# Kernel tuning notes

Hardware: AMD Instinct MI355X
Metric: run time of the kernel (lower is better)

Reference implementation:

```python
import jax, jax.numpy as jnp
import numpy as np
import math

B, S, D, H = 2, 2048, 1024, 16
DK = D // H


def setup_inputs() -> dict:
    key = jax.random.key(0)
    ks = jax.random.split(key, 8)
    s = 1.0 / math.sqrt(D)
    inp = {
        "query": jax.random.normal(ks[0], (B, S, D), jnp.float32),
        "key": jax.random.normal(ks[1], (B, S, D), jnp.float32),
        "value": jax.random.normal(ks[2], (B, S, D), jnp.float32),
        # causal mask: (1, 1, S, S), 1 where attention allowed
        "mask": jnp.tril(jnp.ones((S, S), jnp.int32))[None, None, :, :],
        "Wq": jax.random.normal(ks[3], (D, D), jnp.float32) * s,
        "Wk": jax.random.normal(ks[4], (D, D), jnp.float32) * s,
        "Wv": jax.random.normal(ks[5], (D, D), jnp.float32) * s,
        "Wo": jax.random.normal(ks[6], (D, D), jnp.float32) * s,
    }
    return inp


def reference(query, key, value, mask, Wq, Wk, Wv, Wo):
    # nn.Linear(bias=False): y = x @ W.T
    def proj_heads(x, W):
        y = jnp.einsum("bsd,ed->bse", x, W)          # (B,S,D)
        return y.reshape(B, -1, H, DK).transpose(0, 2, 1, 3)  # (B,H,S,DK)

    q = proj_heads(query, Wq)
    k = proj_heads(key, Wk)
    v = proj_heads(value, Wv)

    scale = jnp.asarray(math.sqrt(DK), q.dtype)
    scores = jnp.einsum("bhqd,bhkd->bhqk", q, k) / scale  # (B,H,S,S)
    scores = jnp.where(mask == 0, -jnp.inf, scores)
    attn = jax.nn.softmax(scores, axis=-1)
    # dropout p=0.0 (eval): identity
    out = jnp.einsum("bhqk,bhkd->bhqd", attn, v)          # (B,H,S,DK)
    concat = out.transpose(0, 2, 1, 3).reshape(B, -1, D)  # (B,S,D)
    return jnp.einsum("bsd,ed->bse", concat, Wo)
```

## Files before the change

kernel.cpp:

```cpp
#include <hip/hip_runtime.h>
#include <hip/hip_bf16.h>

#define B_ 2
#define S_ 2048
#define D_ 1024
#define H_ 16
#define DK_ 64

typedef __hip_bfloat16 bf16;
typedef __attribute__((ext_vector_type(8))) short bf16x8;
typedef __attribute__((ext_vector_type(4))) short bf16x4;
typedef __attribute__((ext_vector_type(4))) float f32x4;

#define GLDS16(g, l)                                                     \
    __builtin_amdgcn_global_load_lds(                                    \
        (const __attribute__((address_space(1))) void*)(g),              \
        (__attribute__((address_space(3))) void*)(l), 16, 0, 0)

#define MFMA_K32(a, b, c) __builtin_amdgcn_mfma_f32_16x16x32_bf16(a, b, c, 0, 0, 0)
#define MFMA_K16(a, b, c) __builtin_amdgcn_mfma_f32_16x16x16bf16_1k(a, b, c, 0, 0, 0)
#define EXP2F(x) __builtin_amdgcn_exp2f(x)

__global__ __launch_bounds__(256) void cvt_all(
    const float* __restrict__ q, const float* __restrict__ k, const float* __restrict__ v,
    const float* __restrict__ w0, const float* __restrict__ w1,
    const float* __restrict__ w2, const float* __restrict__ w3,
    bf16* __restrict__ oq, bf16* __restrict__ ok, bf16* __restrict__ ov,
    bf16* __restrict__ o0, bf16* __restrict__ o1, bf16* __restrict__ o2,
    bf16* __restrict__ o3) {
    int bid = blockIdx.x;
    const float* src; bf16* dst; int base;
    if      (bid < 2048) { src = q;  dst = oq; base = bid; }
    else if (bid < 4096) { src = k;  dst = ok; base = bid - 2048; }
    else if (bid < 6144) { src = v;  dst = ov; base = bid - 4096; }
    else if (bid < 6656) { src = w0; dst = o0; base = bid - 6144; }
    else if (bid < 7168) { src = w1; dst = o1; base = bid - 6656; }
    else if (bid < 7680) { src = w2; dst = o2; base = bid - 7168; }
    else                 { src = w3; dst = o3; base = bid - 7680; }
    int i = (base * 256 + threadIdx.x) * 8;
    float4 a = *(const float4*)(src + i);
    float4 b = *(const float4*)(src + i + 4);
    __align__(16) bf16 o[8];
    o[0] = __float2bfloat16(a.x); o[1] = __float2bfloat16(a.y);
    o[2] = __float2bfloat16(a.z); o[3] = __float2bfloat16(a.w);
    o[4] = __float2bfloat16(b.x); o[5] = __float2bfloat16(b.y);
    o[6] = __float2bfloat16(b.z); o[7] = __float2bfloat16(b.w);
    *(bf16x8*)(dst + i) = *(const bf16x8*)o;
}

__device__ __forceinline__ void proj_loop32(const bf16* __restrict__ X,
                                            const bf16* __restrict__ W,
                                            int m0, int n0, bf16* As, bf16* Bs,
                                            f32x4 (&acc)[4][4]) {
    const int K = D_;
    const int tid = threadIdx.x;
    const int lane = tid & 63, wave = tid >> 6;
    const int lm = lane & 15, quad = lane >> 4;
    const int wr = wave >> 1, wc = wave & 1;

    auto stage = [&](int t, int bf) {
        int k0 = t * 32;
        bf16* Ab = As + bf * (128 * 32);
        bf16* Bb = Bs + bf * (128 * 32);
#pragma unroll
        for (int i = 0; i < 2; ++i) {
            int s = i * 256 + tid;
            int row = s >> 2, c = (s & 3) ^ (row & 3);
            GLDS16(X + (size_t)(m0 + row) * K + k0 + c * 8, Ab + s * 8);
        }
#pragma unroll
        for (int i = 0; i < 2; ++i) {
            int s = i * 256 + tid;
            int row = s >> 2, c = (s & 3) ^ (row & 3);
            GLDS16(W + (size_t)(n0 + row) * K + k0 + c * 8, Bb + s * 8);
        }
    };

    stage(0, 0);
    for (int t = 0; t < K / 32; ++t) {
        __syncthreads();
        if (t + 1 < K / 32) stage(t + 1, (t + 1) & 1);
        const bf16* Ab = As + (t & 1) * (128 * 32);
        const bf16* Bb = Bs + (t & 1) * (128 * 32);
        bf16x8 aF[4], bF[4];
#pragma unroll
        for (int mt = 0; mt < 4; ++mt) {
            int row = wr * 64 + mt * 16 + lm;
            aF[mt] = *(const bf16x8*)(Ab + row * 32 + ((quad ^ (row & 3)) * 8));
        }
#pragma unroll
        for (int nt = 0; nt < 4; ++nt) {
            int row = wc * 64 + nt * 16 + lm;
            bF[nt] = *(const bf16x8*)(Bb + row * 32 + ((quad ^ (row & 3)) * 8));
        }
#pragma unroll
        for (int mt = 0; mt < 4; ++mt)
#pragma unroll
            for (int nt = 0; nt < 4; ++nt)
                acc[mt][nt] = MFMA_K32(aF[mt], bF[nt], acc[mt][nt]);
    }
}

__global__ __launch_bounds__(256) void proj_qkv(
    const bf16* __restrict__ qx, const bf16* __restrict__ kx, const bf16* __restrict__ vx,
    const bf16* __restrict__ wq, const bf16* __restrict__ wk, const bf16* __restrict__ wv,
    bf16* __restrict__ qb, bf16* __restrict__ kb, bf16* __restrict__ vtb) {
    __shared__ __align__(16) bf16 As[2 * 128 * 32];
    __shared__ __align__(16) bf16 Bs[2 * 128 * 32];
    const int L = (int)blockIdx.x;
    const int tile = (L & 7) * 96 + (L >> 3);
    const int z = tile >> 8;
    const int rem = tile & 255;
    const int n0 = (rem & 7) * 128;
    const int m0 = (rem >> 3) * 128;
    const bf16* X = (z == 0) ? qx : (z == 1) ? kx : vx;
    const bf16* W = (z == 0) ? wq : (z == 1) ? wk : wv;
    f32x4 acc[4][4] = {};
    proj_loop32(X, W, m0, n0, As, Bs, acc);

    const int lane = threadIdx.x & 63, wave = threadIdx.x >> 6;
    const int lm = lane & 15, quad = lane >> 4;
    const int wr = wave >> 1, wc = wave & 1;
#pragma unroll
    for (int mt = 0; mt < 4; ++mt) {
        int mbase = m0 + wr * 64 + mt * 16 + quad * 4;
#pragma unroll
        for (int nt = 0; nt < 4; ++nt) {
            int n = n0 + wc * 64 + nt * 16 + lm;
            if (z == 2) {
                int b = mbase >> 11, s = mbase & (S_ - 1);
                unsigned short u[4];
#pragma unroll
                for (int r = 0; r < 4; ++r) {
                    bf16 hv = __float2bfloat16(acc[mt][nt][r]);
                    u[r] = *(unsigned short*)&hv;
                }
                ushort4 pk = {u[0], u[1], u[2], u[3]};
                *(ushort4*)(vtb + ((size_t)(b * 1024 + n) * S_ + s)) = pk;
            } else {
                bf16* Y = z ? kb : qb;
#pragma unroll
                for (int r = 0; r < 4; ++r)
                    Y[(size_t)(mbase + r) * D_ + n] = __float2bfloat16(acc[mt][nt][r]);
            }
        }
    }
}

__global__ __launch_bounds__(256) void proj_o(const bf16* __restrict__ X,
                                              const bf16* __restrict__ W,
                                              float* __restrict__ Y) {
    __shared__ __align__(16) bf16 As[2 * 64 * 32];
    __shared__ __align__(16) bf16 Bs[2 * 128 * 32];
    const int L = (int)blockIdx.x;
    const int tile = (L & 7) * 64 + (L >> 3);
    const int n0 = (tile & 7) * 128;
    const int m0 = (tile >> 3) * 64;

    const int K = D_;
    const int tid = threadIdx.x;
    const int lane = tid & 63, wave = tid >> 6;
    const int lm = lane & 15, quad = lane >> 4;
    const int wr = wave >> 1, wc = wave & 1;

    f32x4 acc[2][4] = {};

    auto stage = [&](int t, int bf) {
        int k0 = t * 32;
        bf16* Ab = As + bf * (64 * 32);
        bf16* Bb = Bs + bf * (128 * 32);
        {
            int s = tid;
            int row = s >> 2, c = (s & 3) ^ (row & 3);
            GLDS16(X + (size_t)(m0 + row) * K + k0 + c * 8, Ab + s * 8);
        }
#pragma unroll
        for (int i = 0; i < 2; ++i) {
            int s = i * 256 + tid;
            int row = s >> 2, c = (s & 3) ^ (row & 3);
            GLDS16(W + (size_t)(n0 + row) * K + k0 + c * 8, Bb + s * 8);
        }
    };

    stage(0, 0);
    for (int t = 0; t < K / 32; ++t) {
        __syncthreads();
        if (t + 1 < K / 32) stage(t + 1, (t + 1) & 1);
        const bf16* Ab = As + (t & 1) * (64 * 32);
        const bf16* Bb = Bs + (t & 1) * (128 * 32);
        bf16x8 aF[2], bF[4];
#pragma unroll
        for (int mt = 0; mt < 2; ++mt) {
            int row = wr * 32 + mt * 16 + lm;
            aF[mt] = *(const bf16x8*)(Ab + row * 32 + ((quad ^ (row & 3)) * 8));
        }
#pragma unroll
        for (int nt = 0; nt < 4; ++nt) {
            int row = wc * 64 + nt * 16 + lm;
            bF[nt] = *(const bf16x8*)(Bb + row * 32 + ((quad ^ (row & 3)) * 8));
        }
#pragma unroll
        for (int mt = 0; mt < 2; ++mt)
#pragma unroll
            for (int nt = 0; nt < 4; ++nt)
                acc[mt][nt] = MFMA_K32(aF[mt], bF[nt], acc[mt][nt]);
    }

#pragma unroll
    for (int mt = 0; mt < 2; ++mt) {
        int mbase = m0 + wr * 32 + mt * 16 + quad * 4;
#pragma unroll
        for (int nt = 0; nt < 4; ++nt) {
            int n = n0 + wc * 64 + nt * 16 + lm;
#pragma unroll
            for (int r = 0; r < 4; ++r)
                Y[(size_t)(mbase + r) * D_ + n] = acc[mt][nt][r];
        }
    }
}

__global__ __launch_bounds__(1024, 4) void attn_kernel(const bf16* __restrict__ Q,
                                                       const bf16* __restrict__ Kb,
                                                       const bf16* __restrict__ VT,
                                                       bf16* __restrict__ O) {
    __shared__ __align__(16) bf16 smem[4 * 128 * 64];
    bf16* ktb0 = smem;
    bf16* vtb0 = smem + 2 * 128 * 64;

    const int tid = threadIdx.x;
    const int lane = tid & 63, wave = tid >> 6;
    const int ws = wave & 7, jh = wave >> 3;
    const int lm = lane & 15, quad = lane >> 4;
    const int f = (int)blockIdx.x;
    const int cls = f & 7;
    const int t = f >> 3;
    const int p = t >> 2;
    const int combo = cls + 8 * (t & 3);
    const int b = combo >> 4, h = combo & 15;
    const int qiA = p, qiB = 15 - p;
    const int q0A = qiA * 128 + ws * 16;
    const int q0B = qiB * 128 + ws * 16;

    const size_t bhoff = (size_t)b * S_ * D_ + (size_t)h * DK_;
    const bf16* vtg = VT + ((size_t)b * 1024 + h * DK_) * S_;

    const bf16* qpA = Q + bhoff + (size_t)(q0A + lm) * D_ + quad * 8;
    bf16x8 aqA0 = *(const bf16x8*)(qpA);
    bf16x8 aqA1 = *(const bf16x8*)(qpA + 32);
    const bf16* qpB = Q + bhoff + (size_t)(q0B + lm) * D_ + quad * 8;
    bf16x8 aqB0 = *(const bf16x8*)(qpB);
    bf16x8 aqB1 = *(const bf16x8*)(qpB + 32);

    f32x4 oaccA[4] = {}, oaccB[4] = {};
    float lsumA = 0.f, lsumB = 0.f;
    const float cexp = 0.125f * 1.44269504f;

    auto stage = [&](int i, int bf) {
        int j0s = i * 128;
        {
            int s = tid;
            int j = s >> 3, c = (s & 7) ^ (j & 7);
            GLDS16(Kb + bhoff + (size_t)(j0s + j) * D_ + c * 8,
                   ktb0 + bf * (128 * 64) + s * 8);
        }
        {
            int s = tid;
            int d = s >> 4, c = (s & 15) ^ (d & 15);
            GLDS16(vtg + (size_t)d * S_ + j0s + c * 8,
                   vtb0 + bf * (64 * 128) + s * 8);
        }
    };

    auto dochunk = [&](bf16x8 bk0, bf16x8 bk1, const bf16x4 (&bv)[4], bool mk,
                       bf16x8 aq0, bf16x8 aq1, f32x4 (&oacc)[4], float& lsum) {
        f32x4 z = {};
        z = MFMA_K32(bk0, aq0, z);
        z = MFMA_K32(bk1, aq1, z);
        bf16x4 pa;
        float rs = 0.f;
#pragma unroll
        for (int r = 0; r < 4; ++r) {
            float pv = EXP2F(z[r] * cexp);
            if (mk && (quad * 4 + r > lm)) pv = 0.f;
            rs += pv;
            bf16 hv = __float2bfloat16(pv);
            pa[r] = *(short*)&hv;
        }
        lsum += rs;
#pragma unroll
        for (int dt = 0; dt < 4; ++dt)
            oacc[dt] = MFMA_K16(pa, bv[dt], oacc[dt]);
    };

    const int nt = qiB + 1;
    stage(0, 0);

    for (int i = 0; i < nt; ++i) {
        __syncthreads();
        if (i + 1 < nt) stage(i + 1, (i + 1) & 1);
        const bf16* ktb = ktb0 + (i & 1) * (128 * 64);
        const bf16* vtl = vtb0 + (i & 1) * (64 * 128);

#pragma unroll
        for (int stl = 0; stl < 4; ++stl) {
            int sg = jh * 4 + stl;
            bool actB = (i < qiB) || (sg <= ws);
            bool mkB  = (i == qiB) && (sg == ws);
            bool actA = (i < qiA) || ((i == qiA) && (sg <= ws));
            bool mkA  = (i == qiA) && (sg == ws);
            if (!actB && !actA) continue;

            int j = sg * 16 + lm;
            bf16x8 bk0 = *(const bf16x8*)(ktb + (((j << 3) | (quad ^ (j & 7))) * 8));
            bf16x8 bk1 = *(const bf16x8*)(ktb + (((j << 3) | ((4 + quad) ^ (j & 7))) * 8));
            bf16x4 bv[4];
#pragma unroll
            for (int dt = 0; dt < 4; ++dt) {
                int d = dt * 16 + lm;
                int cl = sg * 2 + (quad >> 1);
                bv[dt] = *(const bf16x4*)(vtl + d * 128 +
                                          ((cl ^ (d & 15)) * 8 + (quad & 1) * 4));
            }
            if (actB) dochunk(bk0, bk1, bv, mkB, aqB0, aqB1, oaccB, lsumB);
            if (actA) dochunk(bk0, bk1, bv, mkA, aqA0, aqA1, oaccA, lsumA);
        }
    }

    __syncthreads();
    float* red = (float*)smem;
    const int rbase = (ws * 64 + lane) * 17;

    auto reduce_finish = [&](f32x4 (&oacc)[4], float lsum, int q0) {
        if (jh == 1) {
#pragma unroll
            for (int dt = 0; dt < 4; ++dt)
#pragma unroll
                for (int r = 0; r < 4; ++r)
                    red[rbase + dt * 4 + r] = oacc[dt][r];
            red[rbase + 16] = lsum;
        }
        __syncthreads();
        if (jh == 0) {
#pragma unroll
            for (int dt = 0; dt < 4; ++dt)
#pragma unroll
                for (int r = 0; r < 4; ++r)
                    oacc[dt][r] += red[rbase + dt * 4 + r];
            float l = lsum + red[rbase + 16];
            l += __shfl_xor(l, 16, 64);
            l += __shfl_xor(l, 32, 64);
#pragma unroll
            for (int r = 0; r < 4; ++r) {
                float inv = 1.f / __shfl(l, quad * 4 + r, 64);
                int qrow = q0 + quad * 4 + r;
#pragma unroll
                for (int dt = 0; dt < 4; ++dt) {
                    int d = dt * 16 + lm;
                    O[bhoff + (size_t)qrow * D_ + d] =
                        __float2bfloat16(oacc[dt][r] * inv);
                }
            }
        }
        __syncthreads();
    };
    reduce_finish(oaccB, lsumB, q0B);
    reduce_finish(oaccA, lsumA, q0A);
}

extern "C" void kernel_launch(void* const* d_in, const int* in_sizes, int n_in,
                              void* d_out, int out_size, void* d_ws, size_t ws_size,
                              hipStream_t stream) {
    const float* q_in = (const float*)d_in[0];
    const float* k_in = (const float*)d_in[1];
    const float* v_in = (const float*)d_in[2];
    const float* Wq_f = (const float*)d_in[4];
    const float* Wk_f = (const float*)d_in[5];
    const float* Wv_f = (const float*)d_in[6];
    const float* Wo_f = (const float*)d_in[7];
    float* out = (float*)d_out;

    const size_t NEL = (size_t)B_ * S_ * D_;
    const size_t WEL = (size_t)D_ * D_;
    bf16* p = (bf16*)d_ws;
    bf16* qx = p;  p += NEL;
    bf16* kx = p;  p += NEL;
    bf16* vx = p;  p += NEL;
    bf16* wq = p;  p += WEL;
    bf16* wk = p;  p += WEL;
    bf16* wv = p;  p += WEL;
    bf16* wo = p;  p += WEL;
    bf16* qb = p;  p += NEL;
    bf16* kb = p;  p += NEL;
    bf16* vtb = p; p += NEL;
    bf16* cb = p;  p += NEL;

    cvt_all<<<8192, 256, 0, stream>>>(q_in, k_in, v_in, Wq_f, Wk_f, Wv_f, Wo_f,
                                      qx, kx, vx, wq, wk, wv, wo);

    proj_qkv<<<dim3(768), 256, 0, stream>>>(qx, kx, vx, wq, wk, wv, qb, kb, vtb);

    attn_kernel<<<dim3(256), 1024, 0, stream>>>(qb, kb, vtb, cb);

    dim3 gproj(D_ / 128, (B_ * S_) / 128);
    proj_o<<<dim3(512), 256, 0, stream>>>(cb, wo, out);
}
```

Before: 211.7 us.

## Triple-buffer projection GEMM loads with explicit vmcnt waits and raw barriers

The projection GEMM main loop moves from double to triple buffering of its LDS tiles, prefetching two K-steps ahead. Each iteration waits with a partial s_waitcnt vmcnt and a raw s_barrier instead of a full __syncthreads, so loads for the next step can stay in flight while the current tile is consumed. The output projection kernel now shares the templated loop. This adds LDS use per block and relies on the hand-set vmcnt counts matching the number of loads issued per stage.

```diff
diff --git a/kernel.cpp b/kernel.cpp
--- a/kernel.cpp
+++ b/kernel.cpp
@@ -48,10 +48,16 @@
     *(bf16x8*)(dst + i) = *(const bf16x8*)o;
 }
 
-__device__ __forceinline__ void proj_loop32(const bf16* __restrict__ X,
-                                            const bf16* __restrict__ W,
-                                            int m0, int n0, bf16* As, bf16* Bs,
-                                            f32x4 (&acc)[4][4]) {
+template <int MROWS>
+__device__ __forceinline__ void proj_loop(const bf16* __restrict__ X,
+                                          const bf16* __restrict__ W,
+                                          int m0, int n0, bf16* As, bf16* Bs,
+                                          f32x4 (&acc)[MROWS / 32][4]) {
+    constexpr int MT = MROWS / 32;
+    constexpr int ASZ = MROWS * 32;
+    constexpr int BSZ = 128 * 32;
+    constexpr int NA = (MROWS * 4) / 256;
+    constexpr int NT = D_ / 32;
     const int K = D_;
     const int tid = threadIdx.x;
     const int lane = tid & 63, wave = tid >> 6;
@@ -60,10 +66,10 @@
 
     auto stage = [&](int t, int bf) {
         int k0 = t * 32;
-        bf16* Ab = As + bf * (128 * 32);
-        bf16* Bb = Bs + bf * (128 * 32);
-#pragma unroll
-        for (int i = 0; i < 2; ++i) {
+        bf16* Ab = As + bf * ASZ;
+        bf16* Bb = Bs + bf * BSZ;
+#pragma unroll
+        for (int i = 0; i < NA; ++i) {
             int s = i * 256 + tid;
             int row = s >> 2, c = (s & 3) ^ (row & 3);
             GLDS16(X + (size_t)(m0 + row) * K + k0 + c * 8, Ab + s * 8);
@@ -77,15 +83,26 @@
     };
 
     stage(0, 0);
-    for (int t = 0; t < K / 32; ++t) {
-        __syncthreads();
-        if (t + 1 < K / 32) stage(t + 1, (t + 1) & 1);
-        const bf16* Ab = As + (t & 1) * (128 * 32);
-        const bf16* Bb = Bs + (t & 1) * (128 * 32);
-        bf16x8 aF[4], bF[4];
-#pragma unroll
-        for (int mt = 0; mt < 4; ++mt) {
-            int row = wr * 64 + mt * 16 + lm;
+    stage(1, 1);
+    for (int t = 0; t < NT; ++t) {
+        if (t + 1 < NT) {
+            if constexpr (MROWS == 128) {
+                asm volatile("s_waitcnt vmcnt(4)" ::: "memory");
+            } else {
+                asm volatile("s_waitcnt vmcnt(3)" ::: "memory");
+            }
+        } else {
+            asm volatile("s_waitcnt vmcnt(0)" ::: "memory");
+        }
+        __builtin_amdgcn_sched_barrier(0);
+        __builtin_amdgcn_s_barrier();
+        if (t + 2 < NT) stage(t + 2, (t + 2) % 3);
+        const bf16* Ab = As + (t % 3) * ASZ;
+        const bf16* Bb = Bs + (t % 3) * BSZ;
+        bf16x8 aF[MT], bF[4];
+#pragma unroll
+        for (int mt = 0; mt < MT; ++mt) {
+            int row = wr * (MROWS / 2) + mt * 16 + lm;
             aF[mt] = *(const bf16x8*)(Ab + row * 32 + ((quad ^ (row & 3)) * 8));
         }
 #pragma unroll
@@ -94,7 +111,7 @@
             bF[nt] = *(const bf16x8*)(Bb + row * 32 + ((quad ^ (row & 3)) * 8));
         }
 #pragma unroll
-        for (int mt = 0; mt < 4; ++mt)
+        for (int mt = 0; mt < MT; ++mt)
 #pragma unroll
             for (int nt = 0; nt < 4; ++nt)
                 acc[mt][nt] = MFMA_K32(aF[mt], bF[nt], acc[mt][nt]);
@@ -105,8 +122,8 @@
     const bf16* __restrict__ qx, const bf16* __restrict__ kx, const bf16* __restrict__ vx,
     const bf16* __restrict__ wq, const bf16* __restrict__ wk, const bf16* __restrict__ wv,
     bf16* __restrict__ qb, bf16* __restrict__ kb, bf16* __restrict__ vtb) {
-    __shared__ __align__(16) bf16 As[2 * 128 * 32];
-    __shared__ __align__(16) bf16 Bs[2 * 128 * 32];
+    __shared__ __align__(16) bf16 As[3 * 128 * 32];
+    __shared__ __align__(16) bf16 Bs[3 * 128 * 32];
     const int L = (int)blockIdx.x;
     const int tile = (L & 7) * 96 + (L >> 3);
     const int z = tile >> 8;
@@ -116,7 +133,7 @@
     const bf16* X = (z == 0) ? qx : (z == 1) ? kx : vx;
     const bf16* W = (z == 0) ? wq : (z == 1) ? wk : wv;
     f32x4 acc[4][4] = {};
-    proj_loop32(X, W, m0, n0, As, Bs, acc);
+    proj_loop<128>(X, W, m0, n0, As, Bs, acc);
 
     const int lane = threadIdx.x & 63, wave = threadIdx.x >> 6;
     const int lm = lane & 15, quad = lane >> 4;
@@ -150,62 +167,18 @@
 __global__ __launch_bounds__(256) void proj_o(const bf16* __restrict__ X,
                                               const bf16* __restrict__ W,
                                               float* __restrict__ Y) {
-    __shared__ __align__(16) bf16 As[2 * 64 * 32];
-    __shared__ __align__(16) bf16 Bs[2 * 128 * 32];
+    __shared__ __align__(16) bf16 As[3 * 64 * 32];
+    __shared__ __align__(16) bf16 Bs[3 * 128 * 32];
     const int L = (int)blockIdx.x;
     const int tile = (L & 7) * 64 + (L >> 3);
     const int n0 = (tile & 7) * 128;
     const int m0 = (tile >> 3) * 64;
-
-    const int K = D_;
-    const int tid = threadIdx.x;
-    const int lane = tid & 63, wave = tid >> 6;
+    f32x4 acc[2][4] = {};
+    proj_loop<64>(X, W, m0, n0, As, Bs, acc);
+
+    const int lane = threadIdx.x & 63, wave = threadIdx.x >> 6;
     const int lm = lane & 15, quad = lane >> 4;
     const int wr = wave >> 1, wc = wave & 1;
-
-    f32x4 acc[2][4] = {};
-
-    auto stage = [&](int t, int bf) {
-        int k0 = t * 32;
-        bf16* Ab = As + bf * (64 * 32);
-        bf16* Bb = Bs + bf * (128 * 32);
-        {
-            int s = tid;
-            int row = s >> 2, c = (s & 3) ^ (row & 3);
-            GLDS16(X + (size_t)(m0 + row) * K + k0 + c * 8, Ab + s * 8);
-        }
-#pragma unroll
-        for (int i = 0; i < 2; ++i) {
-            int s = i * 256 + tid;
-            int row = s >> 2, c = (s & 3) ^ (row & 3);
-            GLDS16(W + (size_t)(n0 + row) * K + k0 + c * 8, Bb + s * 8);
-        }
-    };
-
-    stage(0, 0);
-    for (int t = 0; t < K / 32; ++t) {
-        __syncthreads();
-        if (t + 1 < K / 32) stage(t + 1, (t + 1) & 1);
-        const bf16* Ab = As + (t & 1) * (64 * 32);
-        const bf16* Bb = Bs + (t & 1) * (128 * 32);
-        bf16x8 aF[2], bF[4];
-#pragma unroll
-        for (int mt = 0; mt < 2; ++mt) {
-            int row = wr * 32 + mt * 16 + lm;
-            aF[mt] = *(const bf16x8*)(Ab + row * 32 + ((quad ^ (row & 3)) * 8));
-        }
-#pragma unroll
-        for (int nt = 0; nt < 4; ++nt) {
-            int row = wc * 64 + nt * 16 + lm;
-            bF[nt] = *(const bf16x8*)(Bb + row * 32 + ((quad ^ (row & 3)) * 8));
-        }
-#pragma unroll
-        for (int mt = 0; mt < 2; ++mt)
-#pragma unroll
-            for (int nt = 0; nt < 4; ++nt)
-                acc[mt][nt] = MFMA_K32(aF[mt], bF[nt], acc[mt][nt]);
-    }
-
 #pragma unroll
     for (int mt = 0; mt < 2; ++mt) {
         int mbase = m0 + wr * 32 + mt * 16 + quad * 4;
@@ -401,6 +374,5 @@
 
     attn_kernel<<<dim3(256), 1024, 0, stream>>>(qb, kb, vtb, cb);
 
-    dim3 gproj(D_ / 128, (B_ * S_) / 128);
     proj_o<<<dim3(512), 256, 0, stream>>>(cb, wo, out);
 }
```

Result: slower. 221.6 us (+4.7%).

## Fuse fp32-to-bf16 conversion into QKV projection loads and attention prologue

Applied to the files above, without the earlier changes.

Removes the separate cvt_all kernel. The QKV projection now reads fp32 inputs and weights directly through register-staged loads, converts them to bf16 and writes them into LDS, replacing the global_load_lds DMA path. The Wo conversion moves into the attention kernel prologue, where 256 blocks of 1024 threads cover the 1M weight elements. This saves a launch and the bf16 round-trip through global memory, at the cost of doubled fp32 read bytes per GEMM tile (reread across N-tiles) and register-staged rather than async LDS loads.

```diff
diff --git a/kernel.cpp b/kernel.cpp
--- a/kernel.cpp
+++ b/kernel.cpp
@@ -21,89 +21,18 @@
 #define MFMA_K16(a, b, c) __builtin_amdgcn_mfma_f32_16x16x16bf16_1k(a, b, c, 0, 0, 0)
 #define EXP2F(x) __builtin_amdgcn_exp2f(x)
 
-__global__ __launch_bounds__(256) void cvt_all(
-    const float* __restrict__ q, const float* __restrict__ k, const float* __restrict__ v,
-    const float* __restrict__ w0, const float* __restrict__ w1,
-    const float* __restrict__ w2, const float* __restrict__ w3,
-    bf16* __restrict__ oq, bf16* __restrict__ ok, bf16* __restrict__ ov,
-    bf16* __restrict__ o0, bf16* __restrict__ o1, bf16* __restrict__ o2,
-    bf16* __restrict__ o3) {
-    int bid = blockIdx.x;
-    const float* src; bf16* dst; int base;
-    if      (bid < 2048) { src = q;  dst = oq; base = bid; }
-    else if (bid < 4096) { src = k;  dst = ok; base = bid - 2048; }
-    else if (bid < 6144) { src = v;  dst = ov; base = bid - 4096; }
-    else if (bid < 6656) { src = w0; dst = o0; base = bid - 6144; }
-    else if (bid < 7168) { src = w1; dst = o1; base = bid - 6656; }
-    else if (bid < 7680) { src = w2; dst = o2; base = bid - 7168; }
-    else                 { src = w3; dst = o3; base = bid - 7680; }
-    int i = (base * 256 + threadIdx.x) * 8;
-    float4 a = *(const float4*)(src + i);
-    float4 b = *(const float4*)(src + i + 4);
-    __align__(16) bf16 o[8];
-    o[0] = __float2bfloat16(a.x); o[1] = __float2bfloat16(a.y);
-    o[2] = __float2bfloat16(a.z); o[3] = __float2bfloat16(a.w);
-    o[4] = __float2bfloat16(b.x); o[5] = __float2bfloat16(b.y);
-    o[6] = __float2bfloat16(b.z); o[7] = __float2bfloat16(b.w);
-    *(bf16x8*)(dst + i) = *(const bf16x8*)o;
-}
-
-__device__ __forceinline__ void proj_loop32(const bf16* __restrict__ X,
-                                            const bf16* __restrict__ W,
-                                            int m0, int n0, bf16* As, bf16* Bs,
-                                            f32x4 (&acc)[4][4]) {
-    const int K = D_;
-    const int tid = threadIdx.x;
-    const int lane = tid & 63, wave = tid >> 6;
-    const int lm = lane & 15, quad = lane >> 4;
-    const int wr = wave >> 1, wc = wave & 1;
-
-    auto stage = [&](int t, int bf) {
-        int k0 = t * 32;
-        bf16* Ab = As + bf * (128 * 32);
-        bf16* Bb = Bs + bf * (128 * 32);
-#pragma unroll
-        for (int i = 0; i < 2; ++i) {
-            int s = i * 256 + tid;
-            int row = s >> 2, c = (s & 3) ^ (row & 3);
-            GLDS16(X + (size_t)(m0 + row) * K + k0 + c * 8, Ab + s * 8);
-        }
-#pragma unroll
-        for (int i = 0; i < 2; ++i) {
-            int s = i * 256 + tid;
-            int row = s >> 2, c = (s & 3) ^ (row & 3);
-            GLDS16(W + (size_t)(n0 + row) * K + k0 + c * 8, Bb + s * 8);
-        }
-    };
-
-    stage(0, 0);
-    for (int t = 0; t < K / 32; ++t) {
-        __syncthreads();
-        if (t + 1 < K / 32) stage(t + 1, (t + 1) & 1);
-        const bf16* Ab = As + (t & 1) * (128 * 32);
-        const bf16* Bb = Bs + (t & 1) * (128 * 32);
-        bf16x8 aF[4], bF[4];
-#pragma unroll
-        for (int mt = 0; mt < 4; ++mt) {
-            int row = wr * 64 + mt * 16 + lm;
-            aF[mt] = *(const bf16x8*)(Ab + row * 32 + ((quad ^ (row & 3)) * 8));
-        }
-#pragma unroll
-        for (int nt = 0; nt < 4; ++nt) {
-            int row = wc * 64 + nt * 16 + lm;
-            bF[nt] = *(const bf16x8*)(Bb + row * 32 + ((quad ^ (row & 3)) * 8));
-        }
-#pragma unroll
-        for (int mt = 0; mt < 4; ++mt)
-#pragma unroll
-            for (int nt = 0; nt < 4; ++nt)
-                acc[mt][nt] = MFMA_K32(aF[mt], bF[nt], acc[mt][nt]);
-    }
+__device__ __forceinline__ bf16x8 pack8(float4 a, float4 b) {
+    union { bf16 h[8]; bf16x8 v; } u;
+    u.h[0] = __float2bfloat16(a.x); u.h[1] = __float2bfloat16(a.y);
+    u.h[2] = __float2bfloat16(a.z); u.h[3] = __float2bfloat16(a.w);
+    u.h[4] = __float2bfloat16(b.x); u.h[5] = __float2bfloat16(b.y);
+    u.h[6] = __float2bfloat16(b.z); u.h[7] = __float2bfloat16(b.w);
+    return u.v;
 }
 
 __global__ __launch_bounds__(256) void proj_qkv(
-    const bf16* __restrict__ qx, const bf16* __restrict__ kx, const bf16* __restrict__ vx,
-    const bf16* __restrict__ wq, const bf16* __restrict__ wk, const bf16* __restrict__ wv,
+    const float* __restrict__ qx, const float* __restrict__ kx, const float* __restrict__ vx,
+    const float* __restrict__ wq, const float* __restrict__ wk, const float* __restrict__ wv,
     bf16* __restrict__ qb, bf16* __restrict__ kb, bf16* __restrict__ vtb) {
     __shared__ __align__(16) bf16 As[2 * 128 * 32];
     __shared__ __align__(16) bf16 Bs[2 * 128 * 32];
@@ -113,14 +42,72 @@
     const int rem = tile & 255;
     const int n0 = (rem & 7) * 128;
     const int m0 = (rem >> 3) * 128;
-    const bf16* X = (z == 0) ? qx : (z == 1) ? kx : vx;
-    const bf16* W = (z == 0) ? wq : (z == 1) ? wk : wv;
-    f32x4 acc[4][4] = {};
-    proj_loop32(X, W, m0, n0, As, Bs, acc);
-
-    const int lane = threadIdx.x & 63, wave = threadIdx.x >> 6;
+    const float* X = (z == 0) ? qx : (z == 1) ? kx : vx;
+    const float* W = (z == 0) ? wq : (z == 1) ? wk : wv;
+
+    const int K = D_;
+    const int tid = threadIdx.x;
+    const int lane = tid & 63, wave = tid >> 6;
     const int lm = lane & 15, quad = lane >> 4;
     const int wr = wave >> 1, wc = wave & 1;
+    constexpr int NT = D_ / 32;
+
+    int sA0 = tid,       rA0 = sA0 >> 2, cA0 = (sA0 & 3) ^ (rA0 & 3);
+    int sA1 = 256 + tid, rA1 = sA1 >> 2, cA1 = (sA1 & 3) ^ (rA1 & 3);
+    const float* pa0 = X + (size_t)(m0 + rA0) * K + cA0 * 8;
+    const float* pa1 = X + (size_t)(m0 + rA1) * K + cA1 * 8;
+    const float* pb0 = W + (size_t)(n0 + rA0) * K + cA0 * 8;
+    const float* pb1 = W + (size_t)(n0 + rA1) * K + cA1 * 8;
+
+    float4 ra[4][2];
+
+    auto issue = [&](int t) {
+        int k0 = t * 32;
+        ra[0][0] = *(const float4*)(pa0 + k0); ra[0][1] = *(const float4*)(pa0 + k0 + 4);
+        ra[1][0] = *(const float4*)(pa1 + k0); ra[1][1] = *(const float4*)(pa1 + k0 + 4);
+        ra[2][0] = *(const float4*)(pb0 + k0); ra[2][1] = *(const float4*)(pb0 + k0 + 4);
+        ra[3][0] = *(const float4*)(pb1 + k0); ra[3][1] = *(const float4*)(pb1 + k0 + 4);
+    };
+    auto commit = [&](int bf) {
+        bf16* Ab = As + bf * (128 * 32);
+        bf16* Bb = Bs + bf * (128 * 32);
+        *(bf16x8*)(Ab + sA0 * 8) = pack8(ra[0][0], ra[0][1]);
+        *(bf16x8*)(Ab + sA1 * 8) = pack8(ra[1][0], ra[1][1]);
+        *(bf16x8*)(Bb + sA0 * 8) = pack8(ra[2][0], ra[2][1]);
+        *(bf16x8*)(Bb + sA1 * 8) = pack8(ra[3][0], ra[3][1]);
+    };
+
+    f32x4 acc[4][4] = {};
+
+    issue(0);
+    commit(0);
+    issue(1);
+    for (int t = 0; t < NT; ++t) {
+        __syncthreads();
+        const bf16* Ab = As + (t & 1) * (128 * 32);
+        const bf16* Bb = Bs + (t & 1) * (128 * 32);
+        bf16x8 aF[4], bF[4];
+#pragma unroll
+        for (int mt = 0; mt < 4; ++mt) {
+            int row = wr * 64 + mt * 16 + lm;
+            aF[mt] = *(const bf16x8*)(Ab + row * 32 + ((quad ^ (row & 3)) * 8));
+        }
+#pragma unroll
+        for (int nt = 0; nt < 4; ++nt) {
+            int row = wc * 64 + nt * 16 + lm;
+            bF[nt] = *(const bf16x8*)(Bb + row * 32 + ((quad ^ (row & 3)) * 8));
+        }
+#pragma unroll
+        for (int mt = 0; mt < 4; ++mt)
+#pragma unroll
+            for (int nt = 0; nt < 4; ++nt)
+                acc[mt][nt] = MFMA_K32(aF[mt], bF[nt], acc[mt][nt]);
+        if (t + 1 < NT) {
+            commit((t + 1) & 1);
+            if (t + 2 < NT) issue(t + 2);
+        }
+    }
+
 #pragma unroll
     for (int mt = 0; mt < 4; ++mt) {
         int mbase = m0 + wr * 64 + mt * 16 + quad * 4;
@@ -222,12 +209,24 @@
 __global__ __launch_bounds__(1024, 4) void attn_kernel(const bf16* __restrict__ Q,
                                                        const bf16* __restrict__ Kb,
                                                        const bf16* __restrict__ VT,
-                                                       bf16* __restrict__ O) {
+                                                       bf16* __restrict__ O,
+                                                       const float* __restrict__ Wof,
+                                                       bf16* __restrict__ wo) {
     __shared__ __align__(16) bf16 smem[4 * 128 * 64];
     bf16* ktb0 = smem;
     bf16* vtb0 = smem + 2 * 128 * 64;
 
     const int tid = threadIdx.x;
+
+    {
+        int idx = ((int)blockIdx.x * 1024 + tid) * 4;
+        float4 w = *(const float4*)(Wof + idx);
+        union { bf16 h[4]; bf16x4 v; } u;
+        u.h[0] = __float2bfloat16(w.x); u.h[1] = __float2bfloat16(w.y);
+        u.h[2] = __float2bfloat16(w.z); u.h[3] = __float2bfloat16(w.w);
+        *(bf16x4*)(wo + idx) = u.v;
+    }
+
     const int lane = tid & 63, wave = tid >> 6;
     const int ws = wave & 7, jh = wave >> 3;
     const int lm = lane & 15, quad = lane >> 4;
@@ -382,25 +381,16 @@
     const size_t NEL = (size_t)B_ * S_ * D_;
     const size_t WEL = (size_t)D_ * D_;
     bf16* p = (bf16*)d_ws;
-    bf16* qx = p;  p += NEL;
-    bf16* kx = p;  p += NEL;
-    bf16* vx = p;  p += NEL;
-    bf16* wq = p;  p += WEL;
-    bf16* wk = p;  p += WEL;
-    bf16* wv = p;  p += WEL;
     bf16* wo = p;  p += WEL;
     bf16* qb = p;  p += NEL;
     bf16* kb = p;  p += NEL;
     bf16* vtb = p; p += NEL;
     bf16* cb = p;  p += NEL;
 
-    cvt_all<<<8192, 256, 0, stream>>>(q_in, k_in, v_in, Wq_f, Wk_f, Wv_f, Wo_f,
-                                      qx, kx, vx, wq, wk, wv, wo);
-
-    proj_qkv<<<dim3(768), 256, 0, stream>>>(qx, kx, vx, wq, wk, wv, qb, kb, vtb);
-
-    attn_kernel<<<dim3(256), 1024, 0, stream>>>(qb, kb, vtb, cb);
-
-    dim3 gproj(D_ / 128, (B_ * S_) / 128);
+    proj_qkv<<<dim3(768), 256, 0, stream>>>(q_in, k_in, v_in,
+                                            Wq_f, Wk_f, Wv_f, qb, kb, vtb);
+
+    attn_kernel<<<dim3(256), 1024, 0, stream>>>(qb, kb, vtb, cb, Wo_f, wo);
+
     proj_o<<<dim3(512), 256, 0, stream>>>(cb, wo, out);
 }
```

New measurement: 228.6 us. 8.0% more time.
